# Performance work log

Measured on AMD Instinct MI355X. Metric: run time of the kernel, lower is better.

The kernel has to match this reference:

```python
import jax, jax.numpy as jnp
import numpy as np
from jax import lax

C = 256
B, T = 4, 4
AH, AW = 32, 32
VH, VW = 56, 56
EPS = 1e-5


def _pool_matrix(n_in, n_out):
    # PyTorch adaptive_avg_pool1d semantics per axis
    M = np.zeros((n_out, n_in), np.float32)
    for i in range(n_out):
        s = (i * n_in) // n_out
        e = -((-(i + 1) * n_in) // n_out)  # ceil
        M[i, s:e] = 1.0 / (e - s)
    return jnp.asarray(M)


def _bilinear_matrix(n_in, n_out):
    # PyTorch bilinear, align_corners=False
    scale = n_in / n_out
    M = np.zeros((n_out, n_in), np.float32)
    for i in range(n_out):
        src = (i + 0.5) * scale - 0.5
        src = min(max(src, 0.0), n_in - 1)
        i0 = int(np.floor(src))
        i1 = min(i0 + 1, n_in - 1)
        w1 = src - i0
        M[i, i0] += 1.0 - w1
        M[i, i1] += w1
    return jnp.asarray(M)


def _group_norm1(x, w, b):
    # GroupNorm(1, C): normalize over (C,H,W) per sample, per-channel affine
    mu = jnp.mean(x, axis=(1, 2, 3), keepdims=True)
    var = jnp.mean(jnp.square(x - mu), axis=(1, 2, 3), keepdims=True)
    xn = (x - mu) * lax.rsqrt(var + EPS)
    return xn * w[None, :, None, None] + b[None, :, None, None]


def _dwconv(x, w, pad, dil):
    c = x.shape[1]
    return lax.conv_general_dilated(
        x, w, window_strides=(1, 1), padding=[(pad, pad), (pad, pad)],
        rhs_dilation=(dil, dil), feature_group_count=c,
        dimension_numbers=('NCHW', 'OIHW', 'NCHW'))


def _pwconv(x, w, b):
    return jnp.einsum('oc,bchw->bohw', w, x) + b[None, :, None, None]


def _lkm(x, gn_w, gn_b, dw7, dw3, pw_w, pw_b):
    x = _group_norm1(x, gn_w, gn_b)
    x = _dwconv(x, dw7, pad=3, dil=1) + _dwconv(x, dw3, pad=3, dil=3)
    x = _pwconv(x, pw_w, pw_b)
    return jax.nn.gelu(x, approximate=False)


def setup_inputs() -> dict:
    key = jax.random.key(0)
    ks = jax.random.split(key, 20)
    s = lambda k, shape, scale=0.05: jax.random.normal(k, shape, jnp.float32) * scale
    return {
        'a': jax.random.normal(ks[0], (B, C, AH, AW), jnp.float32),
        'v': jax.random.normal(ks[1], (B * T, C, VH, VW), jnp.float32),
        'a_gn_w': jnp.ones((C,), jnp.float32), 'a_gn_b': jnp.zeros((C,), jnp.float32),
        'a_dw7': s(ks[2], (C, 1, 7, 7)), 'a_dw3': s(ks[3], (C, 1, 3, 3)),
        'a_pw_w': s(ks[4], (C, C)), 'a_pw_b': jnp.zeros((C,), jnp.float32),
        'v_gn_w': jnp.ones((C,), jnp.float32), 'v_gn_b': jnp.zeros((C,), jnp.float32),
        'v_dw7': s(ks[5], (C, 1, 7, 7)), 'v_dw3': s(ks[6], (C, 1, 3, 3)),
        'v_pw_w': s(ks[7], (C, C)), 'v_pw_b': jnp.zeros((C,), jnp.float32),
        'gate_a_w': s(ks[8], (C, C)), 'gate_a_b': jnp.zeros((C,), jnp.float32),
        'gate_v_w': s(ks[9], (C, C)), 'gate_v_b': jnp.zeros((C,), jnp.float32),
        'scale_a': jnp.ones((1,), jnp.float32), 'scale_v': jnp.ones((1,), jnp.float32),
    }


def reference(a, v, a_gn_w, a_gn_b, a_dw7, a_dw3, a_pw_w, a_pw_b,
              v_gn_w, v_gn_b, v_dw7, v_dw3, v_pw_w, v_pw_b,
              gate_a_w, gate_a_b, gate_v_w, gate_v_b, scale_a, scale_v):
    strength_a = strength_v = 1.0
    temp = 1.0
    b = a.shape[0]
    vb, c, vh, vw = v.shape
    t = vb // b
    ah, aw = a.shape[2], a.shape[3]

    a_feat = _lkm(a, a_gn_w, a_gn_b, a_dw7, a_dw3, a_pw_w, a_pw_b)
    v_feat = _lkm(v, v_gn_w, v_gn_b, v_dw7, v_dw3, v_pw_w, v_pw_b)

    v_feat_mean = v_feat.reshape(b, t, c, vh, vw).mean(axis=1) if t > 1 else v_feat

    if (vh, vw) != (ah, aw):
        Ph, Pw = _pool_matrix(vh, ah), _pool_matrix(vw, aw)
        v_for_a = jnp.einsum('oh,bchw,pw->bcop', Ph, v_feat_mean, Pw)
    else:
        v_for_a = v_feat_mean
    gate_a = jax.nn.sigmoid(_pwconv(v_for_a, gate_a_w, gate_a_b) / temp)

    if (ah, aw) != (vh, vw):
        Rh, Rw = _bilinear_matrix(ah, vh), _bilinear_matrix(aw, vw)
        a_for_v = jnp.einsum('oh,bchw,pw->bcop', Rh, a_feat, Rw)
    else:
        a_for_v = a_feat
    gate_v = jax.nn.sigmoid(_pwconv(a_for_v, gate_v_w, gate_v_b) / temp)
    if t > 1:
        gate_v = jnp.broadcast_to(gate_v[:, None], (b, t, c, vh, vw)).reshape(vb, c, vh, vw)

    a_out = a + strength_a * (scale_a[0] * (a_feat * gate_a))
    v_out = v + strength_v * (scale_v[0] * (v_feat * gate_v))
    return (a_out, v_out)
```

## Files before the change

kernel.cpp:

```cpp
#include <hip/hip_runtime.h>
#include <math.h>

#define C_   256
#define B_   4
#define T_   4
#define AH_  32
#define AW_  32
#define VH_  56
#define VW_  56
#define AHW  (AH_*AW_)
#define VHW  (VH_*VW_)
#define NA_  (B_*C_*AHW)
#define NV_  (B_*T_*C_*VHW)
#define NAV_ (B_*C_*VHW)

typedef unsigned short u16;
typedef short s16x8 __attribute__((ext_vector_type(8)));
typedef unsigned short u16x8 __attribute__((ext_vector_type(8)));
typedef unsigned short u16x4 __attribute__((ext_vector_type(4)));
typedef float f32x4 __attribute__((ext_vector_type(4)));

__device__ __forceinline__ u16 f2b(float f) {
  unsigned u = __float_as_uint(f);
  u += 0x7FFFu + ((u >> 16) & 1u);
  return (u16)(u >> 16);
}
__device__ __forceinline__ float b2f(u16 h) {
  return __uint_as_float((unsigned)h << 16);
}
__device__ __forceinline__ float gelu_f(float x) {
  float x2 = x * x;
  float e = __expf(x * (-1.5957691216f - 0.0713548162f * x2));
  return x * __builtin_amdgcn_rcpf(1.f + e);
}
__device__ __forceinline__ float sigmoid_f(float x) {
  return __builtin_amdgcn_rcpf(1.f + __expf(-x));
}

__global__ __launch_bounds__(256) void gn_reduce1m_cvt(
    const float* __restrict__ a, const float* __restrict__ v,
    float* __restrict__ part,
    const float* __restrict__ s0, const float* __restrict__ s1,
    const float* __restrict__ s2, const float* __restrict__ s3,
    u16* __restrict__ wdst)
{
  int bid = blockIdx.x;
  if (bid < 2560) {
    int samp = bid >> 7, chunk = bid & 127;
    const float* x; int per;
    if (samp < 4) { x = a + (size_t)samp * (C_ * AHW); per = (C_ * AHW / 4) / 128; }
    else          { x = v + (size_t)(samp - 4) * (C_ * VHW); per = (C_ * VHW / 4) / 128; }
    const float4* xb = (const float4*)x + (size_t)chunk * per;
    float s = 0.f, s2 = 0.f;
    for (int i = threadIdx.x; i < per; i += 256) {
      float4 q = xb[i];
      s  += q.x + q.y + q.z + q.w;
      s2 += q.x*q.x + q.y*q.y + q.z*q.z + q.w*q.w;
    }
    __shared__ float sh1[256], sh2[256];
    sh1[threadIdx.x] = s; sh2[threadIdx.x] = s2;
    __syncthreads();
    for (int st = 128; st > 0; st >>= 1) {
      if (threadIdx.x < st) {
        sh1[threadIdx.x] += sh1[threadIdx.x + st];
        sh2[threadIdx.x] += sh2[threadIdx.x + st];
      }
      __syncthreads();
    }
    if (threadIdx.x == 0) {
      part[(samp * 128 + chunk) * 2 + 0] = sh1[0];
      part[(samp * 128 + chunk) * 2 + 1] = sh2[0];
    }
  } else {
    bid -= 2560;
    int g = bid >> 5;
    const float* src = (g == 0) ? s0 : (g == 1) ? s1 : (g == 2) ? s2 : s3;
    size_t i = ((size_t)(bid & 31) * 256 + threadIdx.x) * 8;
    float4 v0 = *(const float4*)(src + i);
    float4 v1 = *(const float4*)(src + i + 4);
    u16x8 o = {f2b(v0.x), f2b(v0.y), f2b(v0.z), f2b(v0.w),
               f2b(v1.x), f2b(v1.y), f2b(v1.z), f2b(v1.w)};
    *(u16x8*)(wdst + (size_t)g * 65536 + i) = o;
  }
}

__global__ __launch_bounds__(128) void gn_reduce2m(
    const float* __restrict__ part, float* __restrict__ stats)
{
  int samp = blockIdx.x;
  int t = threadIdx.x;
  __shared__ float sh1[128], sh2[128];
  sh1[t] = part[(samp * 128 + t) * 2 + 0];
  sh2[t] = part[(samp * 128 + t) * 2 + 1];
  __syncthreads();
  for (int st = 64; st > 0; st >>= 1) {
    if (t < st) { sh1[t] += sh1[t + st]; sh2[t] += sh2[t + st]; }
    __syncthreads();
  }
  if (t == 0) {
    float invN = (samp < 4) ? 1.f / (float)(C_ * AHW) : 1.f / (float)(C_ * VHW);
    float mu  = sh1[0] * invN;
    float var = sh2[0] * invN - mu * mu;
    stats[samp * 2 + 0] = mu;
    stats[samp * 2 + 1] = rsqrtf(var + 1e-5f);
  }
}

__global__ __launch_bounds__(256) void gn_dwconv_all(
    const float* __restrict__ xa, const float* __restrict__ xv,
    const float* __restrict__ stats,
    const float* __restrict__ a_gn_w, const float* __restrict__ a_gn_b,
    const float* __restrict__ a_dw7, const float* __restrict__ a_dw3,
    const float* __restrict__ v_gn_w, const float* __restrict__ v_gn_b,
    const float* __restrict__ v_dw7, const float* __restrict__ v_dw3,
    u16* __restrict__ outa, u16* __restrict__ outv)
{
  __shared__ float tile[62 * 64];
  __shared__ float comb[49];
  const int t = threadIdx.x;
  if (blockIdx.x < 1024) {
    constexpr int TH = 38, TW = 38, TWP = 44;
    const int nc = blockIdx.x;
    const int n = nc >> 8, c = nc & 255;
    const float mu = stats[2 * n], rstd = stats[2 * n + 1];
    const float gsc = a_gn_w[c] * rstd;
    const float gsh = a_gn_b[c] - mu * gsc;
    if (t < 49) comb[t] = a_dw7[c * 49 + t];
    __syncthreads();
    if (t < 9) comb[(t / 3) * 21 + (t % 3) * 3] += a_dw3[c * 9 + t];
    const float* xc = xa + (size_t)nc * AHW;
    for (int idx = t; idx < TH * TW; idx += 256) {
      int th = idx / TW, tw = idx - th * TW;
      int h = th - 3, w = tw - 3;
      float val = 0.f;
      if (h >= 0 && h < 32 && w >= 0 && w < 32) val = xc[h * 32 + w] * gsc + gsh;
      tile[th * TWP + tw] = val;
    }
    __syncthreads();
    if (t < 128) {
      const int rg = t >> 3, cq = t & 7;
      const int r0 = rg * 2, w0 = cq * 4;
      float acc[2][4];
      #pragma unroll
      for (int r = 0; r < 2; ++r)
        #pragma unroll
        for (int j = 0; j < 4; ++j) acc[r][j] = 0.f;
      #pragma unroll
      for (int i = 0; i < 8; ++i) {
        const float* row = &tile[(r0 + i) * TWP + w0];
        float4 ra = *(const float4*)(row);
        float4 rb = *(const float4*)(row + 4);
        float2 rc = *(const float2*)(row + 8);
        float rr[10] = {ra.x, ra.y, ra.z, ra.w, rb.x, rb.y, rb.z, rb.w, rc.x, rc.y};
        #pragma unroll
        for (int ky = 0; ky < 7; ++ky) {
          int orow = i - ky;
          if (orow >= 0 && orow < 2) {
            #pragma unroll
            for (int kx = 0; kx < 7; ++kx) {
              float wg = comb[ky * 7 + kx];
              #pragma unroll
              for (int j = 0; j < 4; ++j)
                acc[orow][j] = fmaf(rr[kx + j], wg, acc[orow][j]);
            }
          }
        }
      }
      u16* oc = outa + (size_t)nc * AHW;
      #pragma unroll
      for (int r = 0; r < 2; ++r) {
        u16x4 res = {f2b(acc[r][0]), f2b(acc[r][1]), f2b(acc[r][2]), f2b(acc[r][3])};
        *(u16x4*)&oc[(r0 + r) * 32 + w0] = res;
      }
    }
  } else {
    const int nc = blockIdx.x - 1024;
    const int n = nc >> 8, c = nc & 255;
    const float mu = stats[8 + 2 * n], rstd = stats[8 + 2 * n + 1];
    const float gsc = v_gn_w[c] * rstd;
    const float gsh = v_gn_b[c] - mu * gsc;
    if (t < 49) comb[t] = v_dw7[c * 49 + t];
    __syncthreads();
    if (t < 9) comb[(t / 3) * 21 + (t % 3) * 3] += v_dw3[c * 9 + t];
    const float* xc = xv + (size_t)nc * VHW;
    if (t < 208) {
      int row, q;
      if (t < 96) { int ri = t >> 4; row = (ri < 3) ? ri : ri + 56; q = t & 15; }
      else        { int r = t - 96; row = 3 + (r >> 1); q = (r & 1) ? 15 : 0; }
      int qz = q ^ (row & 7);
      f32x4 z = {0.f, 0.f, 0.f, 0.f};
      *(f32x4*)&tile[row * 64 + qz * 4] = z;
    }
    #pragma unroll
    for (int it = 0; it < 4; ++it) {
      int idx = t + it * 256;
      if (idx < 784) {
        int row = idx / 14, q = idx - row * 14;
        float4 v = *(const float4*)(xc + row * VW_ + q * 4);
        int trow = row + 3;
        int tq = (q + 1) ^ (trow & 7);
        f32x4 sv = {v.x * gsc + gsh, v.y * gsc + gsh,
                    v.z * gsc + gsh, v.w * gsc + gsh};
        *(f32x4*)&tile[trow * 64 + tq * 4] = sv;
      }
    }
    __syncthreads();
    if (t < 196) {
      const int rg = t / 14, cq = t - rg * 14;
      const int r0 = rg * 4;
      float acc[4][4];
      #pragma unroll
      for (int r = 0; r < 4; ++r)
        #pragma unroll
        for (int j = 0; j < 4; ++j) acc[r][j] = 0.f;
      #pragma unroll
      for (int i = 0; i < 10; ++i) {
        int trow = r0 + i;
        const float* rowb = &tile[trow * 64];
        int rz = trow & 7;
        float rr[12];
        #pragma unroll
        for (int k = 0; k < 3; ++k) {
          int qk = (cq + k) ^ rz;
          f32x4 rv = *(const f32x4*)(rowb + qk * 4);
          rr[4 * k + 0] = rv[0]; rr[4 * k + 1] = rv[1];
          rr[4 * k + 2] = rv[2]; rr[4 * k + 3] = rv[3];
        }
        #pragma unroll
        for (int ky = 0; ky < 7; ++ky) {
          int orow = i - ky;
          if (orow >= 0 && orow < 4) {
            #pragma unroll
            for (int kx = 0; kx < 7; ++kx) {
              float wg = comb[ky * 7 + kx];
              #pragma unroll
              for (int j = 0; j < 4; ++j)
                acc[orow][j] = fmaf(rr[j + kx + 1], wg, acc[orow][j]);
            }
          }
        }
      }
      u16* oc = outv + (size_t)nc * VHW;
      #pragma unroll
      for (int r = 0; r < 4; ++r) {
        u16x4 res = {f2b(acc[r][0]), f2b(acc[r][1]), f2b(acc[r][2]), f2b(acc[r][3])};
        *(u16x4*)&oc[(r0 + r) * VW_ + cq * 4] = res;
      }
    }
  }
}

__global__ __launch_bounds__(256) void transpose_all(
    const u16* __restrict__ ina, u16* __restrict__ outa,
    const u16* __restrict__ inv, u16* __restrict__ outv)
{
  __shared__ u16 tile[64 * 68];
  const int t = threadIdx.x;
  int bid = blockIdx.x;
  const u16* in; u16* outp; int HW, PT;
  if (bid < 256) { in = ina; outp = outa; HW = AHW; PT = 16; }
  else           { bid -= 256; in = inv; outp = outv; HW = VHW; PT = 49; }
  int px = bid % PT; int rem = bid / PT;
  int cy = rem & 3, s = rem >> 2;
  const int p0 = px * 64, c0 = cy * 64;
  const u16* src = in + ((size_t)s * 256 + c0) * HW + p0;
  #pragma unroll
  for (int it = 0; it < 2; ++it) {
    int slot = it * 256 + t;
    int cr = slot >> 3, ch = slot & 7;
    u16x8 v = *(const u16x8*)(src + (size_t)cr * HW + ch * 8);
    u16x4 lo = {v[0], v[1], v[2], v[3]}, hi = {v[4], v[5], v[6], v[7]};
    *(u16x4*)&tile[cr * 68 + ch * 8] = lo;
    *(u16x4*)&tile[cr * 68 + ch * 8 + 4] = hi;
  }
  __syncthreads();
  int pr = t >> 2, ch = t & 3;
  u16* dst = outp + ((size_t)s * HW + p0 + pr) * 256 + c0;
  #pragma unroll
  for (int jj = 0; jj < 2; ++jj) {
    int cb = ch * 8 + jj * 32;
    u16x8 o;
    #pragma unroll
    for (int j = 0; j < 8; ++j) o[j] = tile[(cb + j) * 68 + pr];
    *(u16x8*)(dst + cb) = o;
  }
}

template<int ACT, int WPC, int WCP, int NBA, int PTA, int PTV>
__global__ __launch_bounds__(256) void mfma_pw2(
    const u16* __restrict__ Xa, const u16* __restrict__ Wa,
    const float* __restrict__ ba, u16* __restrict__ outa_pc, u16* __restrict__ outa_cp,
    const u16* __restrict__ Xv, const u16* __restrict__ Wv,
    const float* __restrict__ bv, u16* __restrict__ outv_pc, u16* __restrict__ outv_cp)
{
  __shared__ __align__(16) char smem[(256 * 72 + 64 * 72) * 2];
  u16* Wl = (u16*)smem;
  u16* Xl = (u16*)smem + 256 * 72;
  float* Tt = (float*)smem;
  u16*  Pc = (u16*)smem;
  const int t = threadIdx.x;
  const int lane = t & 63, wid = t >> 6;
  const int g = lane >> 4, lr = lane & 15;
  int bid = blockIdx.x;
  const u16 *X, *W; const float* bias; u16 *out_pc, *out_cp; int HW, px, s;
  if (bid < NBA) {
    X = Xa; W = Wa; bias = ba; out_pc = outa_pc; out_cp = outa_cp;
    HW = PTA * 64; px = bid % PTA; s = bid / PTA;
  } else {
    bid -= NBA;
    X = Xv; W = Wv; bias = bv; out_pc = outv_pc; out_cp = outv_cp;
    HW = PTV * 64; px = bid % PTV; s = bid / PTV;
  }
  const int p0 = px * 64;
  const u16* Xs = X + ((size_t)s * HW + p0) * 256;
  f32x4 acc[4][4] = {};
  u16x8 stw[8], stx[2];
  #pragma unroll
  for (int it = 0; it < 8; ++it) {
    int slot = it * 256 + t, row = slot >> 3, ch = slot & 7;
    stw[it] = *(const u16x8*)(W + row * 256 + ch * 8);
  }
  #pragma unroll
  for (int it = 0; it < 2; ++it) {
    int slot = it * 256 + t, row = slot >> 3, ch = slot & 7;
    stx[it] = *(const u16x8*)(Xs + (size_t)row * 256 + ch * 8);
  }
  for (int kt = 0; kt < 4; ++kt) {
    __syncthreads();
    #pragma unroll
    for (int it = 0; it < 8; ++it) {
      int slot = it * 256 + t, row = slot >> 3, ch = slot & 7;
      *(u16x8*)&Wl[row * 72 + ch * 8] = stw[it];
    }
    #pragma unroll
    for (int it = 0; it < 2; ++it) {
      int slot = it * 256 + t, row = slot >> 3, ch = slot & 7;
      *(u16x8*)&Xl[row * 72 + ch * 8] = stx[it];
    }
    __syncthreads();
    if (kt < 3) {
      const int k1 = (kt + 1) * 64;
      #pragma unroll
      for (int it = 0; it < 8; ++it) {
        int slot = it * 256 + t, row = slot >> 3, ch = slot & 7;
        stw[it] = *(const u16x8*)(W + row * 256 + k1 + ch * 8);
      }
      #pragma unroll
      for (int it = 0; it < 2; ++it) {
        int slot = it * 256 + t, row = slot >> 3, ch = slot & 7;
        stx[it] = *(const u16x8*)(Xs + (size_t)row * 256 + k1 + ch * 8);
      }
    }
    #pragma unroll
    for (int ks = 0; ks < 2; ++ks) {
      s16x8 af[4], bf[4];
      #pragma unroll
      for (int m = 0; m < 4; ++m) {
        int row = wid * 64 + m * 16 + lr;
        af[m] = *(const s16x8*)&Wl[row * 72 + ks * 32 + g * 8];
      }
      #pragma unroll
      for (int n = 0; n < 4; ++n) {
        int row = n * 16 + lr;
        bf[n] = *(const s16x8*)&Xl[row * 72 + ks * 32 + g * 8];
      }
      #pragma unroll
      for (int m = 0; m < 4; ++m)
        #pragma unroll
        for (int n = 0; n < 4; ++n)
          acc[m][n] = __builtin_amdgcn_mfma_f32_16x16x32_bf16(af[m], bf[n], acc[m][n], 0, 0, 0);
    }
  }
  __syncthreads();
  #pragma unroll
  for (int m = 0; m < 4; ++m) {
    int ob = wid * 64 + m * 16 + g * 4;
    float4 b4 = *(const float4*)&bias[ob];
    float bb[4] = {b4.x, b4.y, b4.z, b4.w};
    #pragma unroll
    for (int n = 0; n < 4; ++n)
      #pragma unroll
      for (int r = 0; r < 4; ++r) {
        float y = acc[m][n][r] + bb[r];
        acc[m][n][r] = (ACT == 0) ? gelu_f(y) : sigmoid_f(y);
      }
  }
  if (WPC) {
    #pragma unroll
    for (int m = 0; m < 4; ++m) {
      int obase = wid * 64 + m * 16 + g * 4;
      #pragma unroll
      for (int n = 0; n < 4; ++n) {
        int p = n * 16 + lr;
        int op = obase ^ ((p & 7) << 3);
        u16x4 pk = {f2b(acc[m][n][0]), f2b(acc[m][n][1]), f2b(acc[m][n][2]), f2b(acc[m][n][3])};
        *(u16x4*)&Pc[p * 256 + op] = pk;
      }
    }
    __syncthreads();
    int pr = t >> 2;
    u16* dst = out_pc + ((size_t)s * HW + p0 + pr) * 256;
    #pragma unroll
    for (int j = 0; j < 8; ++j) {
      int o = (j * 4 + (t & 3)) * 8;
      int op = o ^ ((pr & 7) << 3);
      u16x8 vv = *(const u16x8*)&Pc[pr * 256 + op];
      *(u16x8*)(dst + o) = vv;
    }
  }
  if (WCP) {
    #pragma unroll
    for (int ho = 0; ho < 2; ++ho) {
      __syncthreads();
      if ((wid >> 1) == ho) {
        #pragma unroll
        for (int m = 0; m < 4; ++m) {
          int ol = (wid & 1) * 64 + m * 16 + g * 4;
          #pragma unroll
          for (int n = 0; n < 4; ++n) {
            int p = n * 16 + lr, q = p >> 2;
            #pragma unroll
            for (int r = 0; r < 4; ++r) {
              int orow = ol + r;
              Tt[orow * 64 + ((q ^ (orow & 15)) << 2) + (p & 3)] = acc[m][n][r];
            }
          }
        }
      }
      __syncthreads();
      #pragma unroll
      for (int it = 0; it < 8; ++it) {
        int slot = it * 256 + t;
        int ol = slot >> 4, q = slot & 15;
        float4 v4 = *(const float4*)&Tt[ol * 64 + ((q ^ (ol & 15)) << 2)];
        u16x4 pk = {f2b(v4.x), f2b(v4.y), f2b(v4.z), f2b(v4.w)};
        int o = ho * 128 + ol;
        *(u16x4*)(out_cp + ((size_t)s * 256 + o) * HW + p0 + q * 4) = pk;
      }
    }
  }
}

__global__ __launch_bounds__(256) void pool_bilin(
    const u16* __restrict__ vf, u16* __restrict__ vfa,
    const u16* __restrict__ af, u16* __restrict__ afv)
{
  int c = threadIdx.x;
  int pb = blockIdx.x;
  if (pb < 4096) {
    int ow = pb & 31, oh = (pb >> 5) & 31, b = pb >> 10;
    int sh = (oh * VH_) >> 5, eh = ((oh + 1) * VH_ + 31) >> 5;
    int sw = (ow * VW_) >> 5, ew = ((ow + 1) * VW_ + 31) >> 5;
    float acc = 0.f;
    for (int tt = 0; tt < T_; ++tt)
      for (int ih = sh; ih < eh; ++ih)
        for (int iw = sw; iw < ew; ++iw)
          acc += b2f(vf[((size_t)(b * T_ + tt) * VHW + ih * VW_ + iw) * 256 + c]);
    vfa[(size_t)pb * 256 + c] = f2b(acc / (float)(T_ * (eh - sh) * (ew - sw)));
  } else {
    pb -= 4096;
    int ow = pb % VW_; int tmp = pb / VW_; int oh = tmp % VH_; int b = tmp / VH_;
    const float sc = (float)AH_ / (float)VH_;
    float srh = fminf(fmaxf((oh + 0.5f) * sc - 0.5f, 0.f), (float)(AH_ - 1));
    float srw = fminf(fmaxf((ow + 0.5f) * sc - 0.5f, 0.f), (float)(AW_ - 1));
    int h0 = (int)srh, w0 = (int)srw;
    int h1 = min(h0 + 1, AH_ - 1), w1 = min(w0 + 1, AW_ - 1);
    float fh = srh - (float)h0, fw = srw - (float)w0;
    const u16* base = af + (size_t)b * AHW * 256 + c;
    float v00 = b2f(base[(h0 * AW_ + w0) * 256]), v01 = b2f(base[(h0 * AW_ + w1) * 256]);
    float v10 = b2f(base[(h1 * AW_ + w0) * 256]), v11 = b2f(base[(h1 * AW_ + w1) * 256]);
    float top = v00 + (v01 - v00) * fw;
    float bot = v10 + (v11 - v10) * fw;
    afv[(size_t)pb * 256 + c] = f2b(top + (bot - top) * fh);
  }
}

__global__ __launch_bounds__(256) void final_av(
    const float* __restrict__ a, const u16* __restrict__ afcp,
    const u16* __restrict__ gacp, const float* __restrict__ sa,
    const float* __restrict__ v, const u16* __restrict__ vfcp,
    const u16* __restrict__ gvcp, const float* __restrict__ sv,
    float* __restrict__ out)
{
  int bid = blockIdx.x;
  if (bid < 512) {
    size_t i = ((size_t)bid * 256 + threadIdx.x) * 8;
    float s = sa[0];
    float4 a0 = *(const float4*)(a + i), a1 = *(const float4*)(a + i + 4);
    u16x8 f = *(const u16x8*)(afcp + i);
    u16x8 gg = *(const u16x8*)(gacp + i);
    float4 o0 = {a0.x + s * b2f(f[0]) * b2f(gg[0]), a0.y + s * b2f(f[1]) * b2f(gg[1]),
                 a0.z + s * b2f(f[2]) * b2f(gg[2]), a0.w + s * b2f(f[3]) * b2f(gg[3])};
    float4 o1 = {a1.x + s * b2f(f[4]) * b2f(gg[4]), a1.y + s * b2f(f[5]) * b2f(gg[5]),
                 a1.z + s * b2f(f[6]) * b2f(gg[6]), a1.w + s * b2f(f[7]) * b2f(gg[7])};
    *(float4*)(out + i) = o0;
    *(float4*)(out + i + 4) = o1;
  } else {
    size_t i = ((size_t)(bid - 512) * 256 + threadIdx.x) * 8;
    const size_t PER = (size_t)C_ * VHW;
    int bt = (int)(i / PER);
    size_t rem = i - (size_t)bt * PER;
    const u16* gp = gvcp + (size_t)(bt >> 2) * PER + rem;
    float s = sv[0];
    float4 v0 = *(const float4*)(v + i), v1 = *(const float4*)(v + i + 4);
    u16x8 f = *(const u16x8*)(vfcp + i);
    u16x8 gg = *(const u16x8*)gp;
    float4 o0 = {v0.x + s * b2f(f[0]) * b2f(gg[0]), v0.y + s * b2f(f[1]) * b2f(gg[1]),
                 v0.z + s * b2f(f[2]) * b2f(gg[2]), v0.w + s * b2f(f[3]) * b2f(gg[3])};
    float4 o1 = {v1.x + s * b2f(f[4]) * b2f(gg[4]), v1.y + s * b2f(f[5]) * b2f(gg[5]),
                 v1.z + s * b2f(f[6]) * b2f(gg[6]), v1.w + s * b2f(f[7]) * b2f(gg[7])};
    float* ov = out + NA_;
    *(float4*)(ov + i) = o0;
    *(float4*)(ov + i + 4) = o1;
  }
}

extern "C" void kernel_launch(void* const* d_in, const int* in_sizes, int n_in,
                              void* d_out, int out_size, void* d_ws, size_t ws_size,
                              hipStream_t stream)
{
  const float* a        = (const float*)d_in[0];
  const float* v        = (const float*)d_in[1];
  const float* a_gn_w   = (const float*)d_in[2];
  const float* a_gn_b   = (const float*)d_in[3];
  const float* a_dw7    = (const float*)d_in[4];
  const float* a_dw3    = (const float*)d_in[5];
  const float* a_pw_w   = (const float*)d_in[6];
  const float* a_pw_b   = (const float*)d_in[7];
  const float* v_gn_w   = (const float*)d_in[8];
  const float* v_gn_b   = (const float*)d_in[9];
  const float* v_dw7    = (const float*)d_in[10];
  const float* v_dw3    = (const float*)d_in[11];
  const float* v_pw_w   = (const float*)d_in[12];
  const float* v_pw_b   = (const float*)d_in[13];
  const float* gate_a_w = (const float*)d_in[14];
  const float* gate_a_b = (const float*)d_in[15];
  const float* gate_v_w = (const float*)d_in[16];
  const float* gate_v_b = (const float*)d_in[17];
  const float* scale_a  = (const float*)d_in[18];
  const float* scale_v  = (const float*)d_in[19];
  float* out = (float*)d_out;
  char* wsb = (char*)d_ws;

  const size_t SZ_V  = (size_t)NV_ * 2;
  const size_t SZ_AV = (size_t)NAV_ * 2;
  const size_t SZ_A  = (size_t)NA_ * 2;
  u16* dwv_b    = (u16*)(wsb + 0);
  u16* vfeat_cp = (u16*)(wsb + 0);
  u16* dwvT     = (u16*)(wsb + SZ_V);
  u16* afv      = (u16*)(wsb + SZ_V);
  u16* gatev_cp = (u16*)(wsb + SZ_V + SZ_AV);
  u16* vfeat_pc = (u16*)(wsb + 2 * SZ_V);
  u16* dwa_b    = (u16*)(wsb + 3 * SZ_V);
  u16* dwaT     = (u16*)(wsb + 3 * SZ_V + SZ_A);
  u16* afeat_pc = (u16*)(wsb + 3 * SZ_V + 2 * SZ_A);
  u16* afeat_cp = (u16*)(wsb + 3 * SZ_V + 3 * SZ_A);
  u16* vfa      = (u16*)(wsb + 3 * SZ_V + 4 * SZ_A);
  u16* gatea_cp = (u16*)(wsb + 3 * SZ_V + 5 * SZ_A);
  u16* w_bf     = (u16*)(wsb + 3 * SZ_V + 6 * SZ_A);
  float* pf     = (float*)(wsb + 3 * SZ_V + 6 * SZ_A + 4 * 65536 * 2);
  float* part   = pf;
  float* stats  = pf + 5120;
  u16* wA = w_bf, *wV = w_bf + 65536, *wGA = w_bf + 131072, *wGV = w_bf + 196608;

  gn_reduce1m_cvt<<<2688, 256, 0, stream>>>(a, v, part,
      a_pw_w, v_pw_w, gate_a_w, gate_v_w, w_bf);
  gn_reduce2m<<<20, 128, 0, stream>>>(part, stats);

  gn_dwconv_all<<<5120, 256, 0, stream>>>(a, v, stats,
      a_gn_w, a_gn_b, a_dw7, a_dw3, v_gn_w, v_gn_b, v_dw7, v_dw3, dwa_b, dwv_b);

  transpose_all<<<3392, 256, 0, stream>>>(dwa_b, dwaT, dwv_b, dwvT);

  mfma_pw2<0, 1, 1, 64, 16, 49><<<848, 256, 0, stream>>>(
      dwaT, wA, a_pw_b, afeat_pc, afeat_cp,
      dwvT, wV, v_pw_b, vfeat_pc, vfeat_cp);

  pool_bilin<<<16640, 256, 0, stream>>>(vfeat_pc, vfa, afeat_pc, afv);

  mfma_pw2<1, 0, 1, 64, 16, 49><<<260, 256, 0, stream>>>(
      vfa, wGA, gate_a_b, nullptr, gatea_cp,
      afv, wGV, gate_v_b, nullptr, gatev_cp);

  final_av<<<6784, 256, 0, stream>>>(a, afeat_cp, gatea_cp, scale_a,
                                     v, vfeat_cp, gatev_cp, scale_v, out);
}
```

Baseline: 143.4 us.

## Fuse GN stats reduction into dwconv and bilinear upsample into gate GEMM

Removes the separate gn_reduce2m launch: each dwconv block now reduces the 128 partial sums for its sample with wave shuffles. The bilinear upsample of a_feat is computed on the fly inside a new gate GEMM kernel (mfma_gates) while staging the X operand, so the afv intermediate is no longer written and re-read. pool_bilin is reduced to the adaptive-pool path only. This trades two launches and an intermediate buffer round-trip for redundant per-block stat reductions and four gathered loads per staged element in the gate GEMM.

```diff
diff --git a/kernel.cpp b/kernel.cpp
--- a/kernel.cpp
+++ b/kernel.cpp
@@ -84,31 +84,9 @@
   }
 }
 
-__global__ __launch_bounds__(128) void gn_reduce2m(
-    const float* __restrict__ part, float* __restrict__ stats)
-{
-  int samp = blockIdx.x;
-  int t = threadIdx.x;
-  __shared__ float sh1[128], sh2[128];
-  sh1[t] = part[(samp * 128 + t) * 2 + 0];
-  sh2[t] = part[(samp * 128 + t) * 2 + 1];
-  __syncthreads();
-  for (int st = 64; st > 0; st >>= 1) {
-    if (t < st) { sh1[t] += sh1[t + st]; sh2[t] += sh2[t + st]; }
-    __syncthreads();
-  }
-  if (t == 0) {
-    float invN = (samp < 4) ? 1.f / (float)(C_ * AHW) : 1.f / (float)(C_ * VHW);
-    float mu  = sh1[0] * invN;
-    float var = sh2[0] * invN - mu * mu;
-    stats[samp * 2 + 0] = mu;
-    stats[samp * 2 + 1] = rsqrtf(var + 1e-5f);
-  }
-}
-
 __global__ __launch_bounds__(256) void gn_dwconv_all(
     const float* __restrict__ xa, const float* __restrict__ xv,
-    const float* __restrict__ stats,
+    const float* __restrict__ part,
     const float* __restrict__ a_gn_w, const float* __restrict__ a_gn_b,
     const float* __restrict__ a_dw7, const float* __restrict__ a_dw3,
     const float* __restrict__ v_gn_w, const float* __restrict__ v_gn_b,
@@ -117,17 +95,37 @@
 {
   __shared__ float tile[62 * 64];
   __shared__ float comb[49];
+  __shared__ float sstat[2];
   const int t = threadIdx.x;
-  if (blockIdx.x < 1024) {
+  const int apath = (blockIdx.x < 1024);
+  const int nc = apath ? blockIdx.x : (blockIdx.x - 1024);
+  const int n = nc >> 8, c = nc & 255;
+  const int samp = apath ? n : (4 + n);
+  if (t < 64) {
+    float s1 = part[(samp * 128 + t) * 2 + 0] + part[(samp * 128 + 64 + t) * 2 + 0];
+    float s2 = part[(samp * 128 + t) * 2 + 1] + part[(samp * 128 + 64 + t) * 2 + 1];
+    #pragma unroll
+    for (int off = 32; off > 0; off >>= 1) {
+      s1 += __shfl_xor(s1, off);
+      s2 += __shfl_xor(s2, off);
+    }
+    if (t == 0) {
+      float invN = apath ? (1.f / (float)(C_ * AHW)) : (1.f / (float)(C_ * VHW));
+      float mu = s1 * invN;
+      float var = s2 * invN - mu * mu;
+      sstat[0] = mu;
+      sstat[1] = rsqrtf(var + 1e-5f);
+    }
+  }
+  if (t < 49) comb[t] = apath ? a_dw7[c * 49 + t] : v_dw7[c * 49 + t];
+  __syncthreads();
+  if (t < 9) comb[(t / 3) * 21 + (t % 3) * 3] +=
+      apath ? a_dw3[c * 9 + t] : v_dw3[c * 9 + t];
+  const float mu = sstat[0], rstd = sstat[1];
+  if (apath) {
     constexpr int TH = 38, TW = 38, TWP = 44;
-    const int nc = blockIdx.x;
-    const int n = nc >> 8, c = nc & 255;
-    const float mu = stats[2 * n], rstd = stats[2 * n + 1];
     const float gsc = a_gn_w[c] * rstd;
     const float gsh = a_gn_b[c] - mu * gsc;
-    if (t < 49) comb[t] = a_dw7[c * 49 + t];
-    __syncthreads();
-    if (t < 9) comb[(t / 3) * 21 + (t % 3) * 3] += a_dw3[c * 9 + t];
     const float* xc = xa + (size_t)nc * AHW;
     for (int idx = t; idx < TH * TW; idx += 256) {
       int th = idx / TW, tw = idx - th * TW;
@@ -174,14 +172,8 @@
       }
     }
   } else {
-    const int nc = blockIdx.x - 1024;
-    const int n = nc >> 8, c = nc & 255;
-    const float mu = stats[8 + 2 * n], rstd = stats[8 + 2 * n + 1];
     const float gsc = v_gn_w[c] * rstd;
     const float gsh = v_gn_b[c] - mu * gsc;
-    if (t < 49) comb[t] = v_dw7[c * 49 + t];
-    __syncthreads();
-    if (t < 9) comb[(t / 3) * 21 + (t % 3) * 3] += v_dw3[c * 9 + t];
     const float* xc = xv + (size_t)nc * VHW;
     if (t < 208) {
       int row, q;
@@ -441,38 +433,196 @@
   }
 }
 
-__global__ __launch_bounds__(256) void pool_bilin(
-    const u16* __restrict__ vf, u16* __restrict__ vfa,
-    const u16* __restrict__ af, u16* __restrict__ afv)
+__global__ __launch_bounds__(256) void mfma_gates(
+    const u16* __restrict__ Xa, const u16* __restrict__ Wa,
+    const float* __restrict__ ba, u16* __restrict__ outa_cp,
+    const u16* __restrict__ AF, const u16* __restrict__ Wv,
+    const float* __restrict__ bv, u16* __restrict__ outv_cp)
+{
+  __shared__ __align__(16) char smem[(256 * 72 + 64 * 72) * 2];
+  u16* Wl = (u16*)smem;
+  u16* Xl = (u16*)smem + 256 * 72;
+  float* Tt = (float*)smem;
+  const int t = threadIdx.x;
+  const int lane = t & 63, wid = t >> 6;
+  const int g = lane >> 4, lr = lane & 15;
+  int bid = blockIdx.x;
+  const int apath = (bid < 64);
+  const u16* W; const float* bias; u16* out_cp; int HW, px, s;
+  if (apath) {
+    W = Wa; bias = ba; out_cp = outa_cp;
+    HW = AHW; px = bid & 15; s = bid >> 4;
+  } else {
+    bid -= 64;
+    W = Wv; bias = bv; out_cp = outv_cp;
+    HW = VHW; px = bid % 49; s = bid / 49;
+  }
+  const int p0 = px * 64;
+  const u16* Xs = apath ? (Xa + ((size_t)s * HW + p0) * 256) : nullptr;
+  size_t o00[2], o01[2], o10[2], o11[2];
+  float W00[2], W01[2], W10[2], W11[2];
+  const int ch8 = (t & 7) * 8;
+  if (!apath) {
+    #pragma unroll
+    for (int r = 0; r < 2; ++r) {
+      int p = p0 + r * 32 + (t >> 3);
+      int oh = p / 56, ow = p - oh * 56;
+      const float sc = (float)AH_ / (float)VH_;
+      float srh = fminf(fmaxf((oh + 0.5f) * sc - 0.5f, 0.f), 31.f);
+      float srw = fminf(fmaxf((ow + 0.5f) * sc - 0.5f, 0.f), 31.f);
+      int h0 = (int)srh, w0 = (int)srw;
+      int h1 = min(h0 + 1, 31), w1 = min(w0 + 1, 31);
+      float fh = srh - (float)h0, fw = srw - (float)w0;
+      size_t base = (size_t)s * AHW;
+      o00[r] = (base + h0 * 32 + w0) * 256;
+      o01[r] = (base + h0 * 32 + w1) * 256;
+      o10[r] = (base + h1 * 32 + w0) * 256;
+      o11[r] = (base + h1 * 32 + w1) * 256;
+      W00[r] = (1.f - fh) * (1.f - fw); W01[r] = (1.f - fh) * fw;
+      W10[r] = fh * (1.f - fw);         W11[r] = fh * fw;
+    }
+  }
+  f32x4 acc[4][4] = {};
+  u16x8 stw[8], stx[2];
+  #pragma unroll
+  for (int it = 0; it < 8; ++it) {
+    int slot = it * 256 + t, row = slot >> 3, ch = slot & 7;
+    stw[it] = *(const u16x8*)(W + row * 256 + ch * 8);
+  }
+  #pragma unroll
+  for (int it = 0; it < 2; ++it) {
+    if (apath) {
+      int slot = it * 256 + t, row = slot >> 3, ch = slot & 7;
+      stx[it] = *(const u16x8*)(Xs + (size_t)row * 256 + ch * 8);
+    } else {
+      u16x8 a00 = *(const u16x8*)(AF + o00[it] + ch8);
+      u16x8 a01 = *(const u16x8*)(AF + o01[it] + ch8);
+      u16x8 a10 = *(const u16x8*)(AF + o10[it] + ch8);
+      u16x8 a11 = *(const u16x8*)(AF + o11[it] + ch8);
+      u16x8 ox;
+      #pragma unroll
+      for (int j = 0; j < 8; ++j)
+        ox[j] = f2b(W00[it] * b2f(a00[j]) + W01[it] * b2f(a01[j]) +
+                    W10[it] * b2f(a10[j]) + W11[it] * b2f(a11[j]));
+      stx[it] = ox;
+    }
+  }
+  for (int kt = 0; kt < 4; ++kt) {
+    __syncthreads();
+    #pragma unroll
+    for (int it = 0; it < 8; ++it) {
+      int slot = it * 256 + t, row = slot >> 3, ch = slot & 7;
+      *(u16x8*)&Wl[row * 72 + ch * 8] = stw[it];
+    }
+    #pragma unroll
+    for (int it = 0; it < 2; ++it) {
+      int slot = it * 256 + t, row = slot >> 3, ch = slot & 7;
+      *(u16x8*)&Xl[row * 72 + ch * 8] = stx[it];
+    }
+    __syncthreads();
+    if (kt < 3) {
+      const int k1 = (kt + 1) * 64;
+      #pragma unroll
+      for (int it = 0; it < 8; ++it) {
+        int slot = it * 256 + t, row = slot >> 3, ch = slot & 7;
+        stw[it] = *(const u16x8*)(W + row * 256 + k1 + ch * 8);
+      }
+      #pragma unroll
+      for (int it = 0; it < 2; ++it) {
+        if (apath) {
+          int slot = it * 256 + t, row = slot >> 3, ch = slot & 7;
+          stx[it] = *(const u16x8*)(Xs + (size_t)row * 256 + k1 + ch * 8);
+        } else {
+          u16x8 a00 = *(const u16x8*)(AF + o00[it] + k1 + ch8);
+          u16x8 a01 = *(const u16x8*)(AF + o01[it] + k1 + ch8);
+          u16x8 a10 = *(const u16x8*)(AF + o10[it] + k1 + ch8);
+          u16x8 a11 = *(const u16x8*)(AF + o11[it] + k1 + ch8);
+          u16x8 ox;
+          #pragma unroll
+          for (int j = 0; j < 8; ++j)
+            ox[j] = f2b(W00[it] * b2f(a00[j]) + W01[it] * b2f(a01[j]) +
+                        W10[it] * b2f(a10[j]) + W11[it] * b2f(a11[j]));
+          stx[it] = ox;
+        }
+      }
+    }
+    #pragma unroll
+    for (int ks = 0; ks < 2; ++ks) {
+      s16x8 af[4], bf[4];
+      #pragma unroll
+      for (int m = 0; m < 4; ++m) {
+        int row = wid * 64 + m * 16 + lr;
+        af[m] = *(const s16x8*)&Wl[row * 72 + ks * 32 + g * 8];
+      }
+      #pragma unroll
+      for (int n = 0; n < 4; ++n) {
+        int row = n * 16 + lr;
+        bf[n] = *(const s16x8*)&Xl[row * 72 + ks * 32 + g * 8];
+      }
+      #pragma unroll
+      for (int m = 0; m < 4; ++m)
+        #pragma unroll
+        for (int n = 0; n < 4; ++n)
+          acc[m][n] = __builtin_amdgcn_mfma_f32_16x16x32_bf16(af[m], bf[n], acc[m][n], 0, 0, 0);
+    }
+  }
+  __syncthreads();
+  #pragma unroll
+  for (int m = 0; m < 4; ++m) {
+    int ob = wid * 64 + m * 16 + g * 4;
+    float4 b4 = *(const float4*)&bias[ob];
+    float bb[4] = {b4.x, b4.y, b4.z, b4.w};
+    #pragma unroll
+    for (int n = 0; n < 4; ++n)
+      #pragma unroll
+      for (int r = 0; r < 4; ++r)
+        acc[m][n][r] = sigmoid_f(acc[m][n][r] + bb[r]);
+  }
+  #pragma unroll
+  for (int ho = 0; ho < 2; ++ho) {
+    __syncthreads();
+    if ((wid >> 1) == ho) {
+      #pragma unroll
+      for (int m = 0; m < 4; ++m) {
+        int ol = (wid & 1) * 64 + m * 16 + g * 4;
+        #pragma unroll
+        for (int n = 0; n < 4; ++n) {
+          int p = n * 16 + lr, q = p >> 2;
+          #pragma unroll
+          for (int r = 0; r < 4; ++r) {
+            int orow = ol + r;
+            Tt[orow * 64 + ((q ^ (orow & 15)) << 2) + (p & 3)] = acc[m][n][r];
+          }
+        }
+      }
+    }
+    __syncthreads();
+    #pragma unroll
+    for (int it = 0; it < 8; ++it) {
+      int slot = it * 256 + t;
+      int ol = slot >> 4, q = slot & 15;
+      float4 v4 = *(const float4*)&Tt[ol * 64 + ((q ^ (ol & 15)) << 2)];
+      u16x4 pk = {f2b(v4.x), f2b(v4.y), f2b(v4.z), f2b(v4.w)};
+      int o = ho * 128 + ol;
+      *(u16x4*)(out_cp + ((size_t)s * 256 + o) * HW + p0 + q * 4) = pk;
+    }
+  }
+}
+
+__global__ __launch_bounds__(256) void pool_only(
+    const u16* __restrict__ vf, u16* __restrict__ vfa)
 {
   int c = threadIdx.x;
   int pb = blockIdx.x;
-  if (pb < 4096) {
-    int ow = pb & 31, oh = (pb >> 5) & 31, b = pb >> 10;
-    int sh = (oh * VH_) >> 5, eh = ((oh + 1) * VH_ + 31) >> 5;
-    int sw = (ow * VW_) >> 5, ew = ((ow + 1) * VW_ + 31) >> 5;
-    float acc = 0.f;
-    for (int tt = 0; tt < T_; ++tt)
-      for (int ih = sh; ih < eh; ++ih)
-        for (int iw = sw; iw < ew; ++iw)
-          acc += b2f(vf[((size_t)(b * T_ + tt) * VHW + ih * VW_ + iw) * 256 + c]);
-    vfa[(size_t)pb * 256 + c] = f2b(acc / (float)(T_ * (eh - sh) * (ew - sw)));
-  } else {
-    pb -= 4096;
-    int ow = pb % VW_; int tmp = pb / VW_; int oh = tmp % VH_; int b = tmp / VH_;
-    const float sc = (float)AH_ / (float)VH_;
-    float srh = fminf(fmaxf((oh + 0.5f) * sc - 0.5f, 0.f), (float)(AH_ - 1));
-    float srw = fminf(fmaxf((ow + 0.5f) * sc - 0.5f, 0.f), (float)(AW_ - 1));
-    int h0 = (int)srh, w0 = (int)srw;
-    int h1 = min(h0 + 1, AH_ - 1), w1 = min(w0 + 1, AW_ - 1);
-    float fh = srh - (float)h0, fw = srw - (float)w0;
-    const u16* base = af + (size_t)b * AHW * 256 + c;
-    float v00 = b2f(base[(h0 * AW_ + w0) * 256]), v01 = b2f(base[(h0 * AW_ + w1) * 256]);
-    float v10 = b2f(base[(h1 * AW_ + w0) * 256]), v11 = b2f(base[(h1 * AW_ + w1) * 256]);
-    float top = v00 + (v01 - v00) * fw;
-    float bot = v10 + (v11 - v10) * fw;
-    afv[(size_t)pb * 256 + c] = f2b(top + (bot - top) * fh);
-  }
+  int ow = pb & 31, oh = (pb >> 5) & 31, b = pb >> 10;
+  int sh = (oh * VH_) >> 5, eh = ((oh + 1) * VH_ + 31) >> 5;
+  int sw = (ow * VW_) >> 5, ew = ((ow + 1) * VW_ + 31) >> 5;
+  float acc = 0.f;
+  for (int tt = 0; tt < T_; ++tt)
+    for (int ih = sh; ih < eh; ++ih)
+      for (int iw = sw; iw < ew; ++iw)
+        acc += b2f(vf[((size_t)(b * T_ + tt) * VHW + ih * VW_ + iw) * 256 + c]);
+  vfa[(size_t)pb * 256 + c] = f2b(acc / (float)(T_ * (eh - sh) * (ew - sw)));
 }
 
 __global__ __launch_bounds__(256) void final_av(
@@ -548,7 +698,6 @@
   u16* dwv_b    = (u16*)(wsb + 0);
   u16* vfeat_cp = (u16*)(wsb + 0);
   u16* dwvT     = (u16*)(wsb + SZ_V);
-  u16* afv      = (u16*)(wsb + SZ_V);
   u16* gatev_cp = (u16*)(wsb + SZ_V + SZ_AV);
   u16* vfeat_pc = (u16*)(wsb + 2 * SZ_V);
   u16* dwa_b    = (u16*)(wsb + 3 * SZ_V);
@@ -560,14 +709,12 @@
   u16* w_bf     = (u16*)(wsb + 3 * SZ_V + 6 * SZ_A);
   float* pf     = (float*)(wsb + 3 * SZ_V + 6 * SZ_A + 4 * 65536 * 2);
   float* part   = pf;
-  float* stats  = pf + 5120;
   u16* wA = w_bf, *wV = w_bf + 65536, *wGA = w_bf + 131072, *wGV = w_bf + 196608;
 
   gn_reduce1m_cvt<<<2688, 256, 0, stream>>>(a, v, part,
       a_pw_w, v_pw_w, gate_a_w, gate_v_w, w_bf);
-  gn_reduce2m<<<20, 128, 0, stream>>>(part, stats);
-
-  gn_dwconv_all<<<5120, 256, 0, stream>>>(a, v, stats,
+
+  gn_dwconv_all<<<5120, 256, 0, stream>>>(a, v, part,
       a_gn_w, a_gn_b, a_dw7, a_dw3, v_gn_w, v_gn_b, v_dw7, v_dw3, dwa_b, dwv_b);
 
   transpose_all<<<3392, 256, 0, stream>>>(dwa_b, dwaT, dwv_b, dwvT);
@@ -576,11 +723,11 @@
       dwaT, wA, a_pw_b, afeat_pc, afeat_cp,
       dwvT, wV, v_pw_b, vfeat_pc, vfeat_cp);
 
-  pool_bilin<<<16640, 256, 0, stream>>>(vfeat_pc, vfa, afeat_pc, afv);
-
-  mfma_pw2<1, 0, 1, 64, 16, 49><<<260, 256, 0, stream>>>(
-      vfa, wGA, gate_a_b, nullptr, gatea_cp,
-      afv, wGV, gate_v_b, nullptr, gatev_cp);
+  pool_only<<<4096, 256, 0, stream>>>(vfeat_pc, vfa);
+
+  mfma_gates<<<260, 256, 0, stream>>>(
+      vfa, wGA, gate_a_b, gatea_cp,
+      afeat_pc, wGV, gate_v_b, gatev_cp);
 
   final_av<<<6784, 256, 0, stream>>>(a, afeat_cp, gatea_cp, scale_a,
                                      v, vfeat_cp, gatev_cp, scale_v, out);
```

After: 144.9 us. About the same (+1.0%).
